# Kernel optimization log

Hardware: AMD Instinct MI355X
Metric: run time of the kernel (lower is better)

The kernel has to match this reference:

```python
import jax, jax.numpy as jnp
import numpy as np

INPUT_DIM = 1024
OUTPUT_DIM = 1024
NUM_HEADS = 16  # NOTE: torch .split(num_heads) => chunk SIZE = num_heads
N_CHUNKS = OUTPUT_DIM // NUM_HEADS  # 64 effective heads of dim 16
NEG_INF = -1e9


def setup_inputs() -> dict:
    key = jax.random.key(0)
    k1, k2, k3, k4 = jax.random.split(key, 4)
    B, S = 32, 256
    x = jax.random.normal(k1, (B, S, INPUT_DIM), dtype=jnp.float32)
    mask = jnp.ones((B, S), dtype=jnp.float32)
    # xavier-uniform-ish linear weights, torch layout [out, in]
    lim = float(np.sqrt(6.0 / (INPUT_DIM + OUTPUT_DIM)))
    Wq = jax.random.uniform(k2, (OUTPUT_DIM, INPUT_DIM), jnp.float32, -lim, lim)
    Wk = jax.random.uniform(k3, (OUTPUT_DIM, INPUT_DIM), jnp.float32, -lim, lim)
    Wv = jax.random.uniform(k4, (OUTPUT_DIM, INPUT_DIM), jnp.float32, -lim, lim)
    return {"batch_sequence": x, "sequence_mask": mask, "Wq": Wq, "Wk": Wk, "Wv": Wv}


def _split_heads(m):
    # [B,S,D] -> chunks of size NUM_HEADS stacked in dim 0: [C,B,S,H]
    B, S, D = m.shape
    return jnp.transpose(m.reshape(B, S, N_CHUNKS, NUM_HEADS), (2, 0, 1, 3))


def reference(batch_sequence, sequence_mask, Wq, Wk, Wv):
    q = _split_heads(batch_sequence @ Wq.T)  # [C,B,S,H]
    k = _split_heads(batch_sequence @ Wk.T)
    v = _split_heads(batch_sequence @ Wv.T)
    logits = jnp.einsum("cbqh,cbkh->cbqk", q, k) / jnp.sqrt(
        jnp.asarray(OUTPUT_DIM, batch_sequence.dtype)
    )
    mask2d = sequence_mask[:, :, None] * sequence_mask[:, None, :]  # [B,S,S]
    logits = jnp.where(mask2d[None] > 0, logits, NEG_INF)
    w = jax.nn.softmax(logits, axis=-1)
    out = jnp.einsum("cbqk,cbkh->cbqh", w, v)  # [C,B,S,H]
    B, S = batch_sequence.shape[:2]
    return jnp.transpose(out, (1, 2, 0, 3)).reshape(B, S, OUTPUT_DIM)
```

## Files before the change

kernel.cpp:

```cpp
#include <hip/hip_runtime.h>


typedef unsigned short u16;
typedef unsigned int u32;
typedef __attribute__((ext_vector_type(8))) short short8;
typedef __attribute__((ext_vector_type(4))) short short4v;
typedef __attribute__((ext_vector_type(4))) float floatx4;

#if __has_builtin(__builtin_amdgcn_mfma_f32_16x16x16bf16_1k)
#define MFMA16(A, B, C) __builtin_amdgcn_mfma_f32_16x16x16bf16_1k(A, B, C, 0, 0, 0)
#elif __has_builtin(__builtin_amdgcn_mfma_f32_16x16x16_bf16)
#define MFMA16(A, B, C) __builtin_amdgcn_mfma_f32_16x16x16_bf16(A, B, C, 0, 0, 0)
#else
__device__ __forceinline__ floatx4 mfma16_asm(short4v a, short4v b, floatx4 c) {
  floatx4 d;
  asm volatile("v_mfma_f32_16x16x16_bf16 %0, %1, %2, %3"
               : "=v"(d) : "v"(a), "v"(b), "v"(c));
  return d;
}
#define MFMA16(A, B, C) mfma16_asm(A, B, C)
#endif

#if __has_builtin(__builtin_amdgcn_exp2f)
#define EXP2(x) __builtin_amdgcn_exp2f(x)
#else
#define EXP2(x) __expf((x) * 0.6931471805599453f)
#endif

#define QSCALE 0.045084220f

__device__ __forceinline__ u16 f2bf(float f) {
  union { float f; u32 u; } x; x.f = f;
  u32 r = x.u + 0x7fffu + ((x.u >> 16) & 1u);
  return (u16)(r >> 16);
}
__device__ __forceinline__ float bf2f(u16 u) {
  union { u32 u; float f; } x; x.u = ((u32)u) << 16;
  return x.f;
}

__device__ __forceinline__ void gload16(const void* g, void* l) {
  typedef __attribute__((address_space(1))) const unsigned int gq;
  typedef __attribute__((address_space(3))) unsigned int lq;
  __builtin_amdgcn_global_load_lds((gq*)(size_t)g, (lq*)(size_t)l, 16, 0, 0);
}

#define GK 1024
#define QKS 20
#define VTS 264

__global__ __launch_bounds__(256) void cast_all(const float* __restrict__ x,
                                                const float* __restrict__ wq,
                                                const float* __restrict__ wk,
                                                const float* __restrict__ wv,
                                                u16* __restrict__ XB,
                                                u16* __restrict__ WB) {
  int bid = blockIdx.x;
  const float* src; u16* dst; int off;
  if (bid < 8192)       { src = x;  dst = XB;                 off = bid; }
  else if (bid < 9216)  { src = wq; dst = WB;                 off = bid - 8192; }
  else if (bid < 10240) { src = wk; dst = WB + 1024 * 1024;   off = bid - 9216; }
  else                  { src = wv; dst = WB + 2 * 1024 * 1024; off = bid - 10240; }
  int i = (off * 256 + threadIdx.x) * 4;
  float4 v = *(const float4*)(src + i);
  u32 lo = (u32)f2bf(v.x) | ((u32)f2bf(v.y) << 16);
  u32 hi = (u32)f2bf(v.z) | ((u32)f2bf(v.w) << 16);
  uint2 o; o.x = lo; o.y = hi;
  *(uint2*)(dst + i) = o;
}

template <bool MASKED>
__device__ __forceinline__ void attn_loop(const u16* __restrict__ Ks,
                                          const u16* __restrict__ Vt,
                                          const short4v* bq, const float* mqv,
                                          const float* m_s,
                                          floatx4* oacc, floatx4* lacc,
                                          int col, int quad) {
  const short4v ones = {(short)0x3F80, (short)0x3F80, (short)0x3F80, (short)0x3F80};
#pragma unroll 4
  for (int kt = 0; kt < 16; kt++) {
    const int kb = kt * 16;
    short4v ak = *(const short4v*)(Ks + (kb + col) * QKS + quad * 4);
    short4v av = *(const short4v*)(Vt + col * VTS + kb + quad * 4);
    float mk[4];
    if (MASKED) {
#pragma unroll
      for (int i = 0; i < 4; i++) mk[i] = m_s[kb + quad * 4 + i];
    }
#pragma unroll
    for (int qt = 0; qt < 4; qt++) {
      floatx4 z = {0.f, 0.f, 0.f, 0.f};
      floatx4 st = MFMA16(ak, bq[qt], z);
      float e[4];
#pragma unroll
      for (int i = 0; i < 4; i++) {
        e[i] = EXP2(st[i]);
        if (MASKED) e[i] = (mqv[qt] * mk[i] > 0.f) ? e[i] : 0.f;
      }
      union { u32 u[2]; short4v s; } pk;
      pk.u[0] = __builtin_amdgcn_perm(__float_as_uint(e[1]), __float_as_uint(e[0]), 0x07060302u);
      pk.u[1] = __builtin_amdgcn_perm(__float_as_uint(e[3]), __float_as_uint(e[2]), 0x07060302u);
      lacc[qt] = MFMA16(ones, pk.s, lacc[qt]);
      oacc[qt] = MFMA16(av, pk.s, oacc[qt]);
    }
  }
}

__global__ __launch_bounds__(256) void fused_qkv_attn(const u16* __restrict__ XB,
                                                      const u16* __restrict__ WB,
                                                      const float* __restrict__ mask,
                                                      float* __restrict__ out) {
  __shared__ u16 smem[19456];
  __shared__ float m_s[256];

  const int bid = blockIdx.x;
  const int b = bid & 31;
  const int c = bid >> 5;
  const int t = threadIdx.x;
  const int wave = t >> 6;
  const int lane = t & 63;
  const int col = lane & 15;
  const int quad = lane >> 4;

  u16* Xs = smem;
  u16* Ws = smem + 16384;

  float mv = mask[b * 256 + t];
  m_s[t] = mv;
  const int allones = __syncthreads_and(mv > 0.f);

  const int r_loc = lane >> 3;
  const int xb = (lane & 7) ^ r_loc;

  floatx4 acc[4][3] = {};

  const size_t xrow = ((size_t)b * 256 + wave * 64 + r_loc) * GK + xb * 8;
  const int wg0 = wave * 2;
  int wrow0 = 0, wrow1 = 0;
  if (wave < 3) {
    int wr0 = wg0 * 8 + r_loc, wr1 = wr0 + 8;
    wrow0 = (wr0 >> 4) * 1024 + c * 16 + (wr0 & 15);
    wrow1 = (wr1 >> 4) * 1024 + c * 16 + (wr1 & 15);
  }

  for (int k0 = 0; k0 < GK; k0 += 64) {
    __syncthreads();
#pragma unroll
    for (int i = 0; i < 8; i++)
      gload16(XB + xrow + (size_t)i * 8 * GK + k0, Xs + (wave * 64 + i * 8) * 64);
    if (wave < 3) {
      gload16(WB + (size_t)wrow0 * GK + k0 + xb * 8, Ws + (wg0 * 8) * 64);
      gload16(WB + (size_t)wrow1 * GK + k0 + xb * 8, Ws + (wg0 * 8 + 8) * 64);
    }
    __syncthreads();
#pragma unroll
    for (int kk = 0; kk < 2; kk++) {
      const int pos = ((kk * 4 + quad) ^ (lane & 7)) * 8;
      short8 af[4], bf[3];
#pragma unroll
      for (int mt = 0; mt < 4; mt++)
        af[mt] = *(const short8*)(Xs + (wave * 64 + mt * 16 + col) * 64 + pos);
#pragma unroll
      for (int nt = 0; nt < 3; nt++)
        bf[nt] = *(const short8*)(Ws + (nt * 16 + col) * 64 + pos);
#pragma unroll
      for (int mt = 0; mt < 4; mt++)
#pragma unroll
        for (int nt = 0; nt < 3; nt++)
          acc[mt][nt] = __builtin_amdgcn_mfma_f32_16x16x32_bf16(af[mt], bf[nt], acc[mt][nt], 0, 0, 0);
    }
  }

  __syncthreads();
  u16* Qs = smem;
  u16* Ks = smem + 5120;
  u16* Vt = smem + 10240;
  float* l_s = (float*)(smem + 14464);

#pragma unroll
  for (int mt = 0; mt < 4; mt++) {
    const int row = wave * 64 + mt * 16 + quad * 4;
#pragma unroll
    for (int r = 0; r < 4; r++) {
      Qs[(row + r) * QKS + col] = f2bf(acc[mt][0][r] * QSCALE);
      Ks[(row + r) * QKS + col] = f2bf(acc[mt][1][r]);
      Vt[col * VTS + row + r] = f2bf(acc[mt][2][r]);
    }
  }
  __syncthreads();

  const int q0 = wave * 64;

  short4v bq[4];
#pragma unroll
  for (int qt = 0; qt < 4; qt++)
    bq[qt] = *(const short4v*)(Qs + (q0 + qt * 16 + col) * QKS + quad * 4);

  float mqv[4];
#pragma unroll
  for (int qt = 0; qt < 4; qt++) mqv[qt] = m_s[q0 + qt * 16 + col];

  floatx4 oacc[4] = {};
  floatx4 lacc[4] = {};

  if (allones)
    attn_loop<false>(Ks, Vt, bq, mqv, m_s, oacc, lacc, col, quad);
  else
    attn_loop<true>(Ks, Vt, bq, mqv, m_s, oacc, lacc, col, quad);

  __syncthreads();
  float* ot = (float*)smem;

#pragma unroll
  for (int qt = 0; qt < 4; qt++) {
    if (quad == 0) l_s[q0 + qt * 16 + col] = lacc[qt][0];
#pragma unroll
    for (int r = 0; r < 4; r++)
      ot[(quad * 4 + r) * 257 + q0 + qt * 16 + col] = oacc[qt][r];
  }
  __syncthreads();

  float l = l_s[t];
  float* op = out + ((size_t)b * 256 + t) * 1024 + c * 16;
  float o[16];
  if (allones || l > 0.f) {
    float inv = 1.0f / l;
#pragma unroll
    for (int h = 0; h < 16; h++) o[h] = ot[h * 257 + t] * inv;
  } else {
#pragma unroll
    for (int h = 0; h < 16; h++) o[h] = 0.f;
    for (int k = 0; k < 256; k++)
#pragma unroll
      for (int h = 0; h < 16; h++) o[h] += bf2f(Vt[h * VTS + k]);
#pragma unroll
    for (int h = 0; h < 16; h++) o[h] *= (1.0f / 256.0f);
  }
#pragma unroll
  for (int g = 0; g < 4; g++) {
    float4 r;
    r.x = o[g * 4 + 0]; r.y = o[g * 4 + 1]; r.z = o[g * 4 + 2]; r.w = o[g * 4 + 3];
    *(float4*)(op + g * 4) = r;
  }
}

extern "C" void kernel_launch(void* const* d_in, const int* in_sizes, int n_in,
                              void* d_out, int out_size, void* d_ws, size_t ws_size,
                              hipStream_t stream) {
  const float* x    = (const float*)d_in[0];
  const float* mask = (const float*)d_in[1];
  const float* Wq   = (const float*)d_in[2];
  const float* Wk   = (const float*)d_in[3];
  const float* Wv   = (const float*)d_in[4];
  float* out = (float*)d_out;

  u16* XB = (u16*)d_ws;
  u16* WB = XB + (size_t)8192 * 1024;

  cast_all<<<11264, 256, 0, stream>>>(x, Wq, Wk, Wv, XB, WB);
  fused_qkv_attn<<<2048, 256, 0, stream>>>(XB, WB, mask, out);
}
```

Before: 171.7 us.

## Load GEMM operands directly from global into registers with double buffering

```diff
diff --git a/kernel.cpp b/kernel.cpp
--- a/kernel.cpp
+++ b/kernel.cpp
@@ -37,12 +37,6 @@
 __device__ __forceinline__ float bf2f(u16 u) {
   union { u32 u; float f; } x; x.u = ((u32)u) << 16;
   return x.f;
-}
-
-__device__ __forceinline__ void gload16(const void* g, void* l) {
-  typedef __attribute__((address_space(1))) const unsigned int gq;
-  typedef __attribute__((address_space(3))) unsigned int lq;
-  __builtin_amdgcn_global_load_lds((gq*)(size_t)g, (lq*)(size_t)l, 16, 0, 0);
 }
 
 #define GK 1024
@@ -110,7 +104,7 @@
                                                       const u16* __restrict__ WB,
                                                       const float* __restrict__ mask,
                                                       float* __restrict__ out) {
-  __shared__ u16 smem[19456];
+  __shared__ u16 smem[14976];
   __shared__ float m_s[256];
 
   const int bid = blockIdx.x;
@@ -122,56 +116,47 @@
   const int col = lane & 15;
   const int quad = lane >> 4;
 
-  u16* Xs = smem;
-  u16* Ws = smem + 16384;
-
   float mv = mask[b * 256 + t];
   m_s[t] = mv;
   const int allones = __syncthreads_and(mv > 0.f);
 
-  const int r_loc = lane >> 3;
-  const int xb = (lane & 7) ^ r_loc;
+  const u16* Xw = XB + ((size_t)b * 256 + wave * 64) * GK;
+  const int k_l = quad * 8;
+
+  const u16* arow[4];
+#pragma unroll
+  for (int mt = 0; mt < 4; mt++)
+    arow[mt] = Xw + (size_t)(mt * 16 + col) * GK + k_l;
+  const u16* brow[3];
+#pragma unroll
+  for (int nt = 0; nt < 3; nt++)
+    brow[nt] = WB + (size_t)(nt * 1024 + c * 16 + col) * GK + k_l;
 
   floatx4 acc[4][3] = {};
-
-  const size_t xrow = ((size_t)b * 256 + wave * 64 + r_loc) * GK + xb * 8;
-  const int wg0 = wave * 2;
-  int wrow0 = 0, wrow1 = 0;
-  if (wave < 3) {
-    int wr0 = wg0 * 8 + r_loc, wr1 = wr0 + 8;
-    wrow0 = (wr0 >> 4) * 1024 + c * 16 + (wr0 & 15);
-    wrow1 = (wr1 >> 4) * 1024 + c * 16 + (wr1 & 15);
-  }
-
-  for (int k0 = 0; k0 < GK; k0 += 64) {
-    __syncthreads();
-#pragma unroll
-    for (int i = 0; i < 8; i++)
-      gload16(XB + xrow + (size_t)i * 8 * GK + k0, Xs + (wave * 64 + i * 8) * 64);
-    if (wave < 3) {
-      gload16(WB + (size_t)wrow0 * GK + k0 + xb * 8, Ws + (wg0 * 8) * 64);
-      gload16(WB + (size_t)wrow1 * GK + k0 + xb * 8, Ws + (wg0 * 8 + 8) * 64);
-    }
-    __syncthreads();
-#pragma unroll
-    for (int kk = 0; kk < 2; kk++) {
-      const int pos = ((kk * 4 + quad) ^ (lane & 7)) * 8;
-      short8 af[4], bf[3];
-#pragma unroll
-      for (int mt = 0; mt < 4; mt++)
-        af[mt] = *(const short8*)(Xs + (wave * 64 + mt * 16 + col) * 64 + pos);
+  short8 ax[2][4], bx[2][3];
+
+#pragma unroll
+  for (int mt = 0; mt < 4; mt++) ax[0][mt] = *(const short8*)(arow[mt]);
+#pragma unroll
+  for (int nt = 0; nt < 3; nt++) bx[0][nt] = *(const short8*)(brow[nt]);
+
+#pragma unroll 4
+  for (int i = 0; i < 32; i++) {
+    const int cur = i & 1, nxt = cur ^ 1;
+    if (i < 31) {
+      const int kc = (i + 1) * 32;
+#pragma unroll
+      for (int mt = 0; mt < 4; mt++) ax[nxt][mt] = *(const short8*)(arow[mt] + kc);
+#pragma unroll
+      for (int nt = 0; nt < 3; nt++) bx[nxt][nt] = *(const short8*)(brow[nt] + kc);
+    }
+#pragma unroll
+    for (int mt = 0; mt < 4; mt++)
 #pragma unroll
       for (int nt = 0; nt < 3; nt++)
-        bf[nt] = *(const short8*)(Ws + (nt * 16 + col) * 64 + pos);
-#pragma unroll
-      for (int mt = 0; mt < 4; mt++)
-#pragma unroll
-        for (int nt = 0; nt < 3; nt++)
-          acc[mt][nt] = __builtin_amdgcn_mfma_f32_16x16x32_bf16(af[mt], bf[nt], acc[mt][nt], 0, 0, 0);
-    }
-  }
-
-  __syncthreads();
+        acc[mt][nt] = __builtin_amdgcn_mfma_f32_16x16x32_bf16(ax[cur][mt], bx[cur][nt], acc[mt][nt], 0, 0, 0);
+  }
+
   u16* Qs = smem;
   u16* Ks = smem + 5120;
   u16* Vt = smem + 10240;
```

Result: slower. 303.5 us (+76.7%).
